# Performance work log

Measured on AMD Instinct MI355X. Metric: run time of the kernel, lower is better.

The kernel has to match this reference:

```python
import jax, jax.numpy as jnp
import numpy as np

DIM = 1024
D_STATE = 64
D_CONV = 4
EXPAND = 2
HEADDIM = 64
D_INNER = EXPAND * DIM                      # 2048
NHEADS = D_INNER // HEADDIM                 # 32
D_CONV_DIM = D_INNER + 2 * D_STATE          # 2176 (ngroups=1)
D_IN_PROJ = 2 * D_INNER + 2 * D_STATE + NHEADS  # 4256


def setup_inputs() -> dict:
    key = jax.random.key(0)
    ks = jax.random.split(key, 9)
    B, L = 4, 2048
    x = jax.random.normal(ks[0], (B, L, DIM), dtype=jnp.float32)
    in_proj_w = jax.random.normal(ks[1], (D_IN_PROJ, DIM), dtype=jnp.float32) * 0.02
    conv_w = jax.random.normal(ks[2], (D_CONV_DIM, D_CONV), dtype=jnp.float32) * 0.2
    conv_b = jax.random.normal(ks[3], (D_CONV_DIM,), dtype=jnp.float32) * 0.02
    # dt bias from inverse-softplus of dt ~ U(1e-3, 0.1) (mamba2 init)
    dt = jnp.exp(jax.random.uniform(ks[4], (NHEADS,)) * (np.log(0.1) - np.log(1e-3)) + np.log(1e-3))
    dt_bias = (dt + jnp.log(-jnp.expm1(-dt))).astype(jnp.float32)
    A_log = jnp.log(jax.random.uniform(ks[5], (NHEADS,), minval=1.0, maxval=16.0)).astype(jnp.float32)
    D = jnp.ones((NHEADS,), dtype=jnp.float32)
    norm_w = jnp.ones((D_INNER,), dtype=jnp.float32)
    out_proj_w = jax.random.normal(ks[6], (DIM, D_INNER), dtype=jnp.float32) * 0.02
    return {"x": x, "in_proj_w": in_proj_w, "conv_w": conv_w, "conv_b": conv_b,
            "dt_bias": dt_bias, "A_log": A_log, "D": D, "norm_w": norm_w,
            "out_proj_w": out_proj_w}


def _mamba2_fwd(x, in_proj_w, conv_w, conv_b, dt_bias, A_log, D, norm_w, out_proj_w):
    B, L, _ = x.shape
    zxbcdt = jnp.einsum('bld,ed->ble', x, in_proj_w)  # (B,L,4256)
    z = zxbcdt[..., :D_INNER]
    xBC = zxbcdt[..., D_INNER:D_INNER + D_CONV_DIM]
    dt = jax.nn.softplus(zxbcdt[..., D_INNER + D_CONV_DIM:] + dt_bias)  # (B,L,H)
    # causal depthwise conv (kernel D_CONV) + silu
    xp = jnp.pad(xBC, ((0, 0), (D_CONV - 1, 0), (0, 0)))
    conv = conv_b
    for k in range(D_CONV):
        conv = conv + xp[:, k:k + L, :] * conv_w[:, k]
    xBC = jax.nn.silu(conv)
    x_ssm = xBC[..., :D_INNER].reshape(B, L, NHEADS, HEADDIM)
    Bm = xBC[..., D_INNER:D_INNER + D_STATE]          # (B,L,N) ngroups=1
    Cm = xBC[..., D_INNER + D_STATE:]                 # (B,L,N)
    A = -jnp.exp(A_log)                               # (H,)

    def step(h, inp):
        xt, Bt, Ct, dtt = inp                         # (B,H,P),(B,N),(B,N),(B,H)
        dA = jnp.exp(dtt * A)                         # (B,H)
        h = h * dA[:, :, None, None] + (dtt[:, :, None] * xt)[..., None] * Bt[:, None, None, :]
        y = jnp.einsum('bhpn,bn->bhp', h, Ct)
        return h, y

    h0 = jnp.zeros((B, NHEADS, HEADDIM, D_STATE), dtype=x.dtype)
    xs = (jnp.swapaxes(x_ssm, 0, 1), jnp.swapaxes(Bm, 0, 1),
          jnp.swapaxes(Cm, 0, 1), jnp.swapaxes(dt, 0, 1))
    _, ys = jax.lax.scan(step, h0, xs)                # (L,B,H,P)
    y = jnp.swapaxes(ys, 0, 1) + x_ssm * D[None, None, :, None]
    y = y.reshape(B, L, D_INNER)
    # gated RMSNorm (norm_before_gate=False): norm(y * silu(z))
    g = y * jax.nn.silu(z)
    g = g * jax.lax.rsqrt(jnp.mean(g * g, axis=-1, keepdims=True) + 1e-5) * norm_w
    return jnp.einsum('ble,de->bld', g, out_proj_w)


def reference(x, in_proj_w, conv_w, conv_b, dt_bias, A_log, D, norm_w, out_proj_w):
    return _mamba2_fwd(x, in_proj_w, conv_w, conv_b, dt_bias, A_log, D, norm_w, out_proj_w)
```

## Files before the change

kernel.cpp:

```cpp
#include <hip/hip_runtime.h>
#include <stdint.h>

typedef unsigned short ushort_t;
typedef __attribute__((ext_vector_type(4))) float f32x4;
typedef __attribute__((ext_vector_type(8))) short short8;
typedef __attribute__((ext_vector_type(4))) unsigned short us4;

#define L_SEQ   2048
#define NROWS   8192
#define KDIM    1024
#define DINNER  2048
#define NHEADS  32
#define DSTATE  64
#define DCONVD  2176
#define NPROJ   4256
#define NPROJP  4352
#define LDZX    4352
#define NCHUNK  32

__device__ __forceinline__ float bf2f(ushort_t u) {
    union { uint32_t i; float f; } v; v.i = ((uint32_t)u) << 16; return v.f;
}
__device__ __forceinline__ ushort_t f2bf(float f) {
    uint32_t x = __float_as_uint(f);
    x += 0x7FFFu + ((x >> 16) & 1u);
    return (ushort_t)(x >> 16);
}
__device__ __forceinline__ int swzi(int row, int col) {
    return row * 64 + (col ^ ((row & 7) << 3));
}

#define NX4 (NROWS * KDIM / 4)
#define NW4 (NPROJP * KDIM / 4)
#define NO4 (KDIM * DINNER / 4)
__global__ __launch_bounds__(256) void fused_cast_kernel(
    const float* __restrict__ x, const float* __restrict__ w, const float* __restrict__ ow,
    ushort_t* __restrict__ xbf, ushort_t* __restrict__ wbf, ushort_t* __restrict__ owbf) {
    int i = blockIdx.x * 256 + threadIdx.x;
    if (i < NX4) {
        float4 v = ((const float4*)x)[i];
        ushort4 o;
        o.x = f2bf(v.x); o.y = f2bf(v.y); o.z = f2bf(v.z); o.w = f2bf(v.w);
        ((ushort4*)xbf)[i] = o;
    } else if (i < NX4 + NW4) {
        int j = i - NX4;
        int row = (j * 4) >> 10;
        ushort4 o;
        if (row < NPROJ) {
            float4 v = ((const float4*)w)[j];
            o.x = f2bf(v.x); o.y = f2bf(v.y); o.z = f2bf(v.z); o.w = f2bf(v.w);
        } else { o.x = 0; o.y = 0; o.z = 0; o.w = 0; }
        ((ushort4*)wbf)[j] = o;
    } else if (i < NX4 + NW4 + NO4) {
        int j = i - NX4 - NW4;
        float4 v = ((const float4*)ow)[j];
        ushort4 o;
        o.x = f2bf(v.x); o.y = f2bf(v.y); o.z = f2bf(v.z); o.w = f2bf(v.w);
        ((ushort4*)owbf)[j] = o;
    }
}

__device__ __forceinline__ void async16(const void* g, void* l) {
    __builtin_amdgcn_global_load_lds((const __attribute__((address_space(1))) void*)g,
                                     (__attribute__((address_space(3))) void*)l, 16, 0, 0);
}

template<int BM, bool OUT_BF16>
__global__ __launch_bounds__(512, 1) void gemm256_kernel(const ushort_t* __restrict__ Ap,
                                                         const ushort_t* __restrict__ Bp,
                                                         void* __restrict__ Cp,
                                                         const int K, const int ldc,
                                                         const int ntn) {
    constexpr int NAH = BM / 128;
    constexpr int FR  = BM / 32;
    constexpr int NPAN = 2 * (NAH + 2);
    __shared__ ushort_t ldsAll[NPAN * 8192];
    auto ldsA = [&](int d, int h) { return ldsAll + (size_t)(d * (NAH + 2) + h) * 8192; };
    auto ldsB = [&](int d, int h) { return ldsAll + (size_t)(d * (NAH + 2) + NAH + h) * 8192; };

    const int tid = threadIdx.x;
    const int w = tid >> 6, l = tid & 63;
    const int lr = l & 15, lk = l >> 4;
    const int wm = w >> 2, wn = w & 3;

    const int lin = blockIdx.x;
    const int cpx = gridDim.x >> 3;
    const int swz = (lin & 7) * cpx + (lin >> 3);
    const int nt = swz % ntn, mt = swz / ntn;
    const int m0 = mt * BM, n0 = nt * 256;

    const int row0 = tid >> 3,          c0 = (tid & 7) ^ (row0 & 7);
    const int row1 = (512 + tid) >> 3,  c1 = ((512 + tid) & 7) ^ (row1 & 7);

    const int bcol = wn * 64;
    const int bh = bcol >> 7, bw0 = bcol & 127;

    f32x4 acc[FR][4];
    const f32x4 zero = {0.f, 0.f, 0.f, 0.f};
#pragma unroll
    for (int i = 0; i < FR; ++i)
#pragma unroll
        for (int j = 0; j < 4; ++j) acc[i][j] = zero;

    auto stage = [&](int d_, int isB, int h_, int ktn) {
        const ushort_t* gb = (isB ? Bp + (size_t)(n0 + h_ * 128) * K
                                  : Ap + (size_t)(m0 + h_ * 128) * K) + (size_t)ktn * 64;
        ushort_t* lb = isB ? ldsB(d_, h_) : ldsA(d_, h_);
        async16(gb + (size_t)row0 * K + c0 * 8, lb + w * 512);
        async16(gb + (size_t)row1 * K + c1 * 8, lb + 4096 + w * 512);
    };

#define COMPUTE_KS(ks_) do {                                                          \
        short8 af[FR], bfv[4];                                                        \
        _Pragma("unroll")                                                             \
        for (int fr = 0; fr < FR; ++fr) {                                             \
            const int ar = (NAH == 2 ? 0 : wm * 64) + fr * 16 + lr;                   \
            af[fr] = *(const short8*)&Ah[ar * 64 + ((((ks_) * 4 + lk) ^ (ar & 7)) << 3)]; \
        }                                                                             \
        _Pragma("unroll")                                                             \
        for (int fc = 0; fc < 4; ++fc) {                                              \
            const int br = bw0 + fc * 16 + lr;                                        \
            bfv[fc] = *(const short8*)&Bh[br * 64 + ((((ks_) * 4 + lk) ^ (br & 7)) << 3)]; \
        }                                                                             \
        __builtin_amdgcn_s_setprio(1);                                                \
        _Pragma("unroll")                                                             \
        for (int fr = 0; fr < FR; ++fr)                                               \
            _Pragma("unroll")                                                         \
            for (int fc = 0; fc < 4; ++fc)                                            \
                acc[fr][fc] = __builtin_amdgcn_mfma_f32_16x16x32_bf16(                \
                    af[fr], bfv[fc], acc[fr][fc], 0, 0, 0);                           \
        __builtin_amdgcn_s_setprio(0);                                                \
    } while (0)

    stage(0, 0, 0, 0); stage(0, 1, 0, 0);
    if (NAH == 2) stage(0, 0, 1, 0);
    stage(0, 1, 1, 0);

    const int NKT = K >> 6;
    for (int kt = 0; kt < NKT; ++kt) {
        const int d = kt & 1;
        const bool more = (kt + 1 < NKT);
        const ushort_t* Ah = (NAH == 2) ? ldsA(d, wm) : ldsA(d, 0);
        const ushort_t* Bh = ldsB(d, bh);

        if (more) { stage(d ^ 1, 0, 0, kt + 1); stage(d ^ 1, 1, 0, kt + 1); }
        if (more) asm volatile("s_waitcnt vmcnt(4)" ::: "memory");
        else      asm volatile("s_waitcnt vmcnt(0)" ::: "memory");
        __builtin_amdgcn_s_barrier();

        COMPUTE_KS(0);

        if (more) { if (NAH == 2) stage(d ^ 1, 0, 1, kt + 1); stage(d ^ 1, 1, 1, kt + 1); }

        COMPUTE_KS(1);

        __builtin_amdgcn_s_barrier();
    }
#undef COMPUTE_KS

    if constexpr (OUT_BF16 && BM == 256) {
#pragma unroll
        for (int fr2 = 0; fr2 < FR; ++fr2)
#pragma unroll
            for (int fc2 = 0; fc2 < 4; ++fc2) {
                const int lrow = wm * 128 + fr2 * 16 + lk * 4;
                const int lcol = bcol + fc2 * 16 + lr;
#pragma unroll
                for (int r = 0; r < 4; ++r)
                    ldsAll[(lrow + r) * 256 + lcol] = f2bf(acc[fr2][fc2][r]);
            }
        __builtin_amdgcn_s_barrier();
#pragma unroll
        for (int pass = 0; pass < 16; ++pass) {
            const int e = pass * 4096 + tid * 8;
            const int row = e >> 8, col = e & 255;
            short8 v = *(const short8*)&ldsAll[row * 256 + col];
            *(short8*)((ushort_t*)Cp + (size_t)(m0 + row) * ldc + n0 + col) = v;
        }
    } else {
#pragma unroll
        for (int fr2 = 0; fr2 < FR; ++fr2)
#pragma unroll
            for (int fc2 = 0; fc2 < 4; ++fc2) {
                const int col = n0 + bcol + fc2 * 16 + lr;
                const int rowb = m0 + wm * (BM / 2) + fr2 * 16 + lk * 4;
#pragma unroll
                for (int r = 0; r < 4; ++r) {
                    if (OUT_BF16)
                        ((ushort_t*)Cp)[(size_t)(rowb + r) * ldc + col] = f2bf(acc[fr2][fc2][r]);
                    else
                        ((float*)Cp)[(size_t)(rowb + r) * ldc + col] = acc[fr2][fc2][r];
                }
            }
    }
}

__global__ __launch_bounds__(256) void conv_silu_kernel(const ushort_t* __restrict__ zx,
                                                        const float* __restrict__ conv_w,
                                                        const float* __restrict__ conv_b,
                                                        ushort_t* __restrict__ convout) {
    const int idx = blockIdx.x * 256 + threadIdx.x;
    const int row = idx / 272;
    const int c = (idx - row * 272) * 8;
    const int l = row & (L_SEQ - 1);
    float acc[8];
    {
        const float4* bp = (const float4*)(conv_b + c);
        float4 b0 = bp[0], b1 = bp[1];
        acc[0] = b0.x; acc[1] = b0.y; acc[2] = b0.z; acc[3] = b0.w;
        acc[4] = b1.x; acc[5] = b1.y; acc[6] = b1.z; acc[7] = b1.w;
    }
    float wv[8][4];
    {
        const float4* wp = (const float4*)(conv_w + c * 4);
#pragma unroll
        for (int i = 0; i < 8; ++i) {
            float4 t = wp[i];
            wv[i][0] = t.x; wv[i][1] = t.y; wv[i][2] = t.z; wv[i][3] = t.w;
        }
    }
#pragma unroll
    for (int k = 0; k < 4; ++k) {
        const int ll = l - 3 + k;
        if (ll >= 0) {
            short8 v = *(const short8*)(zx + (size_t)(row - 3 + k) * LDZX + DINNER + c);
#pragma unroll
            for (int i = 0; i < 8; ++i)
                acc[i] += bf2f((ushort_t)v[i]) * wv[i][k];
        }
    }
    short8 o;
#pragma unroll
    for (int i = 0; i < 8; ++i) {
        float s = acc[i] / (1.f + expf(-acc[i]));
        o[i] = (short)f2bf(s);
    }
    *(short8*)(convout + (size_t)row * DCONVD + c) = o;
}

__global__ __launch_bounds__(256) void chunk_intra_kernel(
    const ushort_t* __restrict__ cvb, const ushort_t* __restrict__ zx,
    const float* __restrict__ dt_bias,
    const float* __restrict__ A_log, const float* __restrict__ Dvec,
    ushort_t* __restrict__ ybuf, ushort_t* __restrict__ Gbuf,
    float* __restrict__ expPb)
{
    const int c = blockIdx.x, h = blockIdx.y, b = blockIdx.z;
    const int tid = threadIdx.x;
    const int wv = tid >> 6, lane = tid & 63;
    const int lr = lane & 15, lk = lane >> 4;

    __shared__ __align__(16) ushort_t Cs[4096];
    __shared__ __align__(16) ushort_t Bs[4096];
    __shared__ __align__(16) ushort_t Xt[4096];
    __shared__ __align__(16) ushort_t Ss[4096];
    __shared__ __align__(16) ushort_t Bw[4096];
    __shared__ float sP[64], sdt[64], sWf[64];

    const int t4 = tid >> 2, qq = tid & 3;
    const size_t rowg0 = (size_t)b * L_SEQ + c * 64;
    const ushort_t* rowp = cvb + (rowg0 + t4) * DCONVD;

    short8 rb0 = *(const short8*)(rowp + DINNER + qq * 16);
    short8 rb1 = *(const short8*)(rowp + DINNER + qq * 16 + 8);
    short8 rc0 = *(const short8*)(rowp + DINNER + DSTATE + qq * 16);
    short8 rc1 = *(const short8*)(rowp + DINNER + DSTATE + qq * 16 + 8);
    short8 rx0 = *(const short8*)(rowp + h * 64 + qq * 16);
    short8 rx1 = *(const short8*)(rowp + h * 64 + qq * 16 + 8);

    *(short8*)&Cs[swzi(t4, qq * 16)]     = rc0;
    *(short8*)&Cs[swzi(t4, qq * 16 + 8)] = rc1;
    *(short8*)&Bs[swzi(t4, qq * 16)]     = rb0;
    *(short8*)&Bs[swzi(t4, qq * 16 + 8)] = rb1;
#pragma unroll
    for (int k = 0; k < 8; ++k) {
        Xt[swzi(qq * 16 + k, t4)]     = (ushort_t)rx0[k];
        Xt[swzi(qq * 16 + 8 + k, t4)] = (ushort_t)rx1[k];
    }
    if (tid < 64) {
        float dv = bf2f(zx[(rowg0 + tid) * LDZX + (NPROJ - NHEADS) + h]) + dt_bias[h];
        float dt = (dv > 20.f) ? dv : log1pf(expf(dv));
        float A = -__expf(A_log[h]);
        float P = dt * A;
#pragma unroll
        for (int off = 1; off < 64; off <<= 1) {
            float o = __shfl_up(P, off);
            if (tid >= off) P += o;
        }
        sP[tid] = P;
        sdt[tid] = dt;
        float P63 = __shfl(P, 63);
        sWf[tid] = __expf(P63 - P) * dt;
        expPb[(size_t)(b * NHEADS + h) * L_SEQ + c * 64 + tid] = __expf(P);
    }
    __syncthreads();

    {
        const float w = sWf[t4];
#pragma unroll
        for (int k = 0; k < 8; ++k) {
            Bw[swzi(qq * 16 + k, t4)]     = f2bf(bf2f((ushort_t)rb0[k]) * w);
            Bw[swzi(qq * 16 + 8 + k, t4)] = f2bf(bf2f((ushort_t)rb1[k]) * w);
        }
    }

    const float Dh = Dvec[h];
    {
        short8 a0 = *(const short8*)&Cs[swzi(wv * 16 + lr, lk * 8)];
        short8 a1 = *(const short8*)&Cs[swzi(wv * 16 + lr, 32 + lk * 8)];
        f32x4 acc[4];
        const f32x4 zero = {0.f, 0.f, 0.f, 0.f};
#pragma unroll
        for (int nj = 0; nj < 4; ++nj) {
            short8 b0 = *(const short8*)&Bs[swzi(nj * 16 + lr, lk * 8)];
            short8 b1 = *(const short8*)&Bs[swzi(nj * 16 + lr, 32 + lk * 8)];
            acc[nj] = __builtin_amdgcn_mfma_f32_16x16x32_bf16(a0, b0, zero, 0, 0, 0);
            acc[nj] = __builtin_amdgcn_mfma_f32_16x16x32_bf16(a1, b1, acc[nj], 0, 0, 0);
        }
#pragma unroll
        for (int r = 0; r < 4; ++r) {
            const int i = wv * 16 + lk * 4 + r;
            const float Pi = sP[i];
#pragma unroll
            for (int nj = 0; nj < 4; ++nj) {
                const int j = nj * 16 + lr;
                float s = 0.f;
                if (j <= i) s = acc[nj][r] * __expf(Pi - sP[j]) * sdt[j];
                if (j == i) s += Dh;
                Ss[swzi(i, j)] = f2bf(s);
            }
        }
    }
    __syncthreads();

    {
        short8 a0 = *(const short8*)&Ss[swzi(wv * 16 + lr, lk * 8)];
        short8 a1 = *(const short8*)&Ss[swzi(wv * 16 + lr, 32 + lk * 8)];
        const f32x4 zero = {0.f, 0.f, 0.f, 0.f};
#pragma unroll
        for (int np = 0; np < 4; ++np) {
            short8 b0 = *(const short8*)&Xt[swzi(np * 16 + lr, lk * 8)];
            short8 b1 = *(const short8*)&Xt[swzi(np * 16 + lr, 32 + lk * 8)];
            f32x4 acc = __builtin_amdgcn_mfma_f32_16x16x32_bf16(a0, b0, zero, 0, 0, 0);
            acc = __builtin_amdgcn_mfma_f32_16x16x32_bf16(a1, b1, acc, 0, 0, 0);
#pragma unroll
            for (int r = 0; r < 4; ++r) {
                const int i = wv * 16 + lk * 4 + r;
                const int p = np * 16 + lr;
                ybuf[(rowg0 + i) * DINNER + (size_t)h * 64 + p] = f2bf(acc[r]);
            }
        }
    }

    {
        short8 a0 = *(const short8*)&Xt[swzi(wv * 16 + lr, lk * 8)];
        short8 a1 = *(const short8*)&Xt[swzi(wv * 16 + lr, 32 + lk * 8)];
        const f32x4 zero = {0.f, 0.f, 0.f, 0.f};
        const size_t gbase = ((size_t)((b * NHEADS + h) * NCHUNK + c)) << 12;
#pragma unroll
        for (int nt = 0; nt < 4; ++nt) {
            short8 b0 = *(const short8*)&Bw[swzi(nt * 16 + lr, lk * 8)];
            short8 b1 = *(const short8*)&Bw[swzi(nt * 16 + lr, 32 + lk * 8)];
            f32x4 acc = __builtin_amdgcn_mfma_f32_16x16x32_bf16(a0, b0, zero, 0, 0, 0);
            acc = __builtin_amdgcn_mfma_f32_16x16x32_bf16(a1, b1, acc, 0, 0, 0);
#pragma unroll
            for (int r = 0; r < 4; ++r) {
                const int p = wv * 16 + lk * 4 + r;
                const int n = nt * 16 + lr;
                Gbuf[gbase + p * 64 + n] = f2bf(acc[r]);
            }
        }
    }
}

__global__ __launch_bounds__(256) void state_scan_kernel(
    ushort_t* __restrict__ GH, const float* __restrict__ expPb)
{
    const int half = blockIdx.x, h = blockIdx.y, b = blockIdx.z;
    const int bh = b * NHEADS + h;
    const int e0 = half * 2048 + threadIdx.x * 8;
    ushort_t* base = GH + ((size_t)bh << 17);
    const float* ep = expPb + (size_t)bh * L_SEQ;

    float hr[8];
#pragma unroll
    for (int k = 0; k < 8; ++k) hr[k] = 0.f;

    short8 g = *(const short8*)(base + e0);
    float Ec = ep[63];
    for (int c = 0; c < NCHUNK; ++c) {
        short8 gn = g; float En = 0.f;
        if (c + 1 < NCHUNK) {
            gn = *(const short8*)(base + ((size_t)(c + 1) << 12) + e0);
            En = ep[(c + 1) * 64 + 63];
        }
        short8 o;
#pragma unroll
        for (int k = 0; k < 8; ++k) o[k] = (short)f2bf(hr[k]);
        *(short8*)(base + ((size_t)c << 12) + e0) = o;
#pragma unroll
        for (int k = 0; k < 8; ++k) hr[k] = hr[k] * Ec + bf2f((ushort_t)g[k]);
        g = gn; Ec = En;
    }
}

__global__ __launch_bounds__(256) void y_inter_kernel(
    const ushort_t* __restrict__ cvb, const float* __restrict__ expPb,
    const ushort_t* __restrict__ hst, ushort_t* __restrict__ ybuf)
{
    const int c = blockIdx.x + 1, h = blockIdx.y, b = blockIdx.z;
    const int tid = threadIdx.x;
    const int wv = tid >> 6, lane = tid & 63;
    const int lr = lane & 15, lk = lane >> 4;
    const int bh = b * NHEADS + h;

    __shared__ __align__(16) ushort_t Cs[4096];
    __shared__ __align__(16) ushort_t Hp[4096];
    __shared__ float sEp[64];

    const int t4 = tid >> 2, qq = tid & 3;
    const size_t rowg0 = (size_t)b * L_SEQ + c * 64;
    {
        const ushort_t* rp = cvb + (rowg0 + t4) * DCONVD + DINNER + DSTATE + qq * 16;
        *(short8*)&Cs[swzi(t4, qq * 16)]     = *(const short8*)rp;
        *(short8*)&Cs[swzi(t4, qq * 16 + 8)] = *(const short8*)(rp + 8);
        const ushort_t* hr = hst + (((size_t)(bh * NCHUNK + c)) << 12) + t4 * 64 + qq * 16;
        *(short8*)&Hp[swzi(t4, qq * 16)]     = *(const short8*)hr;
        *(short8*)&Hp[swzi(t4, qq * 16 + 8)] = *(const short8*)(hr + 8);
    }
    if (tid < 64) sEp[tid] = expPb[(size_t)bh * L_SEQ + c * 64 + tid];
    __syncthreads();

    short8 a0 = *(const short8*)&Cs[swzi(wv * 16 + lr, lk * 8)];
    short8 a1 = *(const short8*)&Cs[swzi(wv * 16 + lr, 32 + lk * 8)];
    const f32x4 zero = {0.f, 0.f, 0.f, 0.f};
#pragma unroll
    for (int np = 0; np < 4; ++np) {
        short8 b0 = *(const short8*)&Hp[swzi(np * 16 + lr, lk * 8)];
        short8 b1 = *(const short8*)&Hp[swzi(np * 16 + lr, 32 + lk * 8)];
        f32x4 acc = __builtin_amdgcn_mfma_f32_16x16x32_bf16(a0, b0, zero, 0, 0, 0);
        acc = __builtin_amdgcn_mfma_f32_16x16x32_bf16(a1, b1, acc, 0, 0, 0);
#pragma unroll
        for (int r = 0; r < 4; ++r) {
            const int t = wv * 16 + lk * 4 + r;
            const int p = np * 16 + lr;
            ushort_t* yp = &ybuf[(rowg0 + t) * DINNER + (size_t)h * 64 + p];
            *yp = f2bf(bf2f(*yp) + acc[r] * sEp[t]);
        }
    }
}

__global__ __launch_bounds__(256) void gatenorm_kernel(const ushort_t* __restrict__ ybuf,
                                                       const ushort_t* __restrict__ zx,
                                                       const float* __restrict__ norm_w,
                                                       ushort_t* __restrict__ gbuf) {
    const int row = blockIdx.x;
    const int tid = threadIdx.x;
    short8 yv = *(const short8*)(ybuf + (size_t)row * DINNER + tid * 8);
    short8 zv = *(const short8*)(zx + (size_t)row * LDZX + tid * 8);
    float g[8];
    float ss = 0.f;
#pragma unroll
    for (int i = 0; i < 8; ++i) {
        float y = bf2f((ushort_t)yv[i]);
        float z = bf2f((ushort_t)zv[i]);
        float sz = z / (1.f + expf(-z));
        float gg = y * sz;
        g[i] = gg;
        ss += gg * gg;
    }
#pragma unroll
    for (int o = 32; o > 0; o >>= 1) ss += __shfl_xor(ss, o);
    __shared__ float wsum[4];
    if ((tid & 63) == 0) wsum[tid >> 6] = ss;
    __syncthreads();
    float tot = wsum[0] + wsum[1] + wsum[2] + wsum[3];
    float scale = rsqrtf(tot * (1.0f / (float)DINNER) + 1e-5f);
    short8 o8;
#pragma unroll
    for (int i = 0; i < 8; ++i)
        o8[i] = (short)f2bf(g[i] * scale * norm_w[tid * 8 + i]);
    *(short8*)(gbuf + (size_t)row * DINNER + tid * 8) = o8;
}

extern "C" void kernel_launch(void* const* d_in, const int* in_sizes, int n_in,
                              void* d_out, int out_size, void* d_ws, size_t ws_size,
                              hipStream_t stream) {
    const float* x          = (const float*)d_in[0];
    const float* in_proj_w  = (const float*)d_in[1];
    const float* conv_w     = (const float*)d_in[2];
    const float* conv_b     = (const float*)d_in[3];
    const float* dt_bias    = (const float*)d_in[4];
    const float* A_log      = (const float*)d_in[5];
    const float* Dvec       = (const float*)d_in[6];
    const float* norm_w     = (const float*)d_in[7];
    const float* out_proj_w = (const float*)d_in[8];
    float* out = (float*)d_out;

    char* ws = (char*)d_ws;
    size_t off = 0;
    ushort_t* owbf  = (ushort_t*)(ws + off); off += (size_t)KDIM * DINNER * 2;
    ushort_t* zx    = (ushort_t*)(ws + off); off += (size_t)NROWS * LDZX * 2;
    ushort_t* cvb   = (ushort_t*)(ws + off); off += (size_t)NROWS * DCONVD * 2;
    float*    expPb = (float*)(ws + off);    off += (size_t)128 * L_SEQ * 4;
    ushort_t* ybuf  = (ushort_t*)(ws + off); off += (size_t)NROWS * DINNER * 2;
    char* tail = ws + off;
    ushort_t* xbf  = (ushort_t*)tail;
    ushort_t* wbf  = (ushort_t*)(tail + (size_t)NROWS * KDIM * 2);
    ushort_t* Gbuf = (ushort_t*)tail;
    ushort_t* gbuf = (ushort_t*)tail;

    fused_cast_kernel<<<(NX4 + NW4 + NO4) / 256, 256, 0, stream>>>(
        x, in_proj_w, out_proj_w, xbf, wbf, owbf);

    gemm256_kernel<256, true><<<544, 512, 0, stream>>>(xbf, wbf, zx, KDIM, LDZX, 17);

    conv_silu_kernel<<<NROWS * 272 / 256, 256, 0, stream>>>(zx, conv_w, conv_b, cvb);

    chunk_intra_kernel<<<dim3(NCHUNK, NHEADS, 4), 256, 0, stream>>>(
        cvb, zx, dt_bias, A_log, Dvec, ybuf, Gbuf, expPb);
    state_scan_kernel<<<dim3(2, NHEADS, 4), 256, 0, stream>>>(Gbuf, expPb);
    y_inter_kernel<<<dim3(NCHUNK - 1, NHEADS, 4), 256, 0, stream>>>(
        cvb, expPb, Gbuf, ybuf);

    gatenorm_kernel<<<NROWS, 256, 0, stream>>>(ybuf, zx, norm_w, gbuf);

    gemm256_kernel<128, false><<<256, 512, 0, stream>>>(gbuf, owbf, out, DINNER, KDIM, 4);
}
```

Measured before the change: 297.7 us.

## Split GEMM k-step into four barrier-separated phases interleaving loads and MFMAs

Restructures the GEMM main loop into four phases per k-tile. Each phase issues one async global-to-LDS stage, reads half the A fragments (and B fragments when needed), and runs half the MFMAs, with workgroup barriers between phases. The goal is to spread global loads and LDS reads across the compute so that memory traffic and matrix-core work overlap more evenly, in the style of a ping-pong schedule. The cost is many more barriers per iteration. The first wait (vmcnt(2)) also relies on the stage ordering being right.

Result: slower. 308.4 us (+3.6%).

```diff
diff --git a/kernel.cpp b/kernel.cpp
--- a/kernel.cpp
+++ b/kernel.cpp
@@ -73,6 +73,7 @@
                                                          const int ntn) {
     constexpr int NAH = BM / 128;
     constexpr int FR  = BM / 32;
+    constexpr int FRH = FR / 2;
     constexpr int NPAN = 2 * (NAH + 2);
     __shared__ ushort_t ldsAll[NPAN * 8192];
     auto ldsA = [&](int d, int h) { return ldsAll + (size_t)(d * (NAH + 2) + h) * 8192; };
@@ -110,25 +111,29 @@
         async16(gb + (size_t)row1 * K + c1 * 8, lb + 4096 + w * 512);
     };
 
-#define COMPUTE_KS(ks_) do {                                                          \
-        short8 af[FR], bfv[4];                                                        \
+#define READS(frh_, ks_, doB_) do {                                                   \
         _Pragma("unroll")                                                             \
-        for (int fr = 0; fr < FR; ++fr) {                                             \
-            const int ar = (NAH == 2 ? 0 : wm * 64) + fr * 16 + lr;                   \
+        for (int fr = 0; fr < FRH; ++fr) {                                            \
+            const int ar = (NAH == 2 ? 0 : wm * 64) + ((frh_) * FRH + fr) * 16 + lr;  \
             af[fr] = *(const short8*)&Ah[ar * 64 + ((((ks_) * 4 + lk) ^ (ar & 7)) << 3)]; \
         }                                                                             \
-        _Pragma("unroll")                                                             \
-        for (int fc = 0; fc < 4; ++fc) {                                              \
-            const int br = bw0 + fc * 16 + lr;                                        \
-            bfv[fc] = *(const short8*)&Bh[br * 64 + ((((ks_) * 4 + lk) ^ (br & 7)) << 3)]; \
+        if (doB_) {                                                                   \
+            _Pragma("unroll")                                                         \
+            for (int fc = 0; fc < 4; ++fc) {                                          \
+                const int br = bw0 + fc * 16 + lr;                                    \
+                bfv[fc] = *(const short8*)&Bh[br * 64 + ((((ks_) * 4 + lk) ^ (br & 7)) << 3)]; \
+            }                                                                         \
         }                                                                             \
+    } while (0)
+
+#define MFMAS(frh_) do {                                                              \
         __builtin_amdgcn_s_setprio(1);                                                \
         _Pragma("unroll")                                                             \
-        for (int fr = 0; fr < FR; ++fr)                                               \
+        for (int fr = 0; fr < FRH; ++fr)                                              \
             _Pragma("unroll")                                                         \
             for (int fc = 0; fc < 4; ++fc)                                            \
-                acc[fr][fc] = __builtin_amdgcn_mfma_f32_16x16x32_bf16(                \
-                    af[fr], bfv[fc], acc[fr][fc], 0, 0, 0);                           \
+                acc[(frh_) * FRH + fr][fc] = __builtin_amdgcn_mfma_f32_16x16x32_bf16( \
+                    af[fr], bfv[fc], acc[(frh_) * FRH + fr][fc], 0, 0, 0);            \
         __builtin_amdgcn_s_setprio(0);                                                \
     } while (0)
 
@@ -142,21 +147,36 @@
         const bool more = (kt + 1 < NKT);
         const ushort_t* Ah = (NAH == 2) ? ldsA(d, wm) : ldsA(d, 0);
         const ushort_t* Bh = ldsB(d, bh);
-
-        if (more) { stage(d ^ 1, 0, 0, kt + 1); stage(d ^ 1, 1, 0, kt + 1); }
-        if (more) asm volatile("s_waitcnt vmcnt(4)" ::: "memory");
+        short8 af[FRH], bfv[4];
+
+        if (more) stage(d ^ 1, 0, 0, kt + 1);
+        if (more) asm volatile("s_waitcnt vmcnt(2)" ::: "memory");
         else      asm volatile("s_waitcnt vmcnt(0)" ::: "memory");
         __builtin_amdgcn_s_barrier();
-
-        COMPUTE_KS(0);
-
-        if (more) { if (NAH == 2) stage(d ^ 1, 0, 1, kt + 1); stage(d ^ 1, 1, 1, kt + 1); }
-
-        COMPUTE_KS(1);
-
-        __builtin_amdgcn_s_barrier();
-    }
-#undef COMPUTE_KS
+        READS(0, 0, 1);
+        MFMAS(0);
+        __builtin_amdgcn_s_barrier();
+
+        if (more) stage(d ^ 1, 1, 0, kt + 1);
+        READS(1, 0, 0);
+        __builtin_amdgcn_s_barrier();
+        MFMAS(1);
+        __builtin_amdgcn_s_barrier();
+
+        if (more && NAH == 2) stage(d ^ 1, 0, 1, kt + 1);
+        READS(0, 1, 1);
+        __builtin_amdgcn_s_barrier();
+        MFMAS(0);
+        __builtin_amdgcn_s_barrier();
+
+        if (more) stage(d ^ 1, 1, 1, kt + 1);
+        READS(1, 1, 0);
+        __builtin_amdgcn_s_barrier();
+        MFMAS(1);
+        __builtin_amdgcn_s_barrier();
+    }
+#undef READS
+#undef MFMAS
 
     if constexpr (OUT_BF16 && BM == 256) {
 #pragma unroll
```
